# Kernel optimization log

Measured on AMD Instinct MI355X. Metric: run time of the kernel, lower is better.

## Reference

```python
import jax, jax.numpy as jnp
import numpy as np

BETA = 0.25


def setup_inputs() -> dict:
    key = jax.random.key(0)
    k1, k2 = jax.random.split(key)
    z = jax.random.normal(k1, (16, 64, 32, 32), dtype=jnp.float32)
    emb_w = jax.random.normal(k2, (16384, 64), dtype=jnp.float32)
    return {"z": z, "emb_w": emb_w}


def reference(z, emb_w):
    # z: [b, c, h, w] with c == embed_dim; emb_w: [n_embed, embed_dim]
    b, c, h, w = z.shape
    zc = jnp.transpose(z, (0, 2, 3, 1))          # [b, h, w, c]
    zf = zc.reshape(-1, c)                        # [N, c]
    # squared euclidean distances: ||z||^2 - 2 z E^T + ||E||^2  -> [N, n_embed]
    d = (jnp.sum(zf * zf, axis=1, keepdims=True)
         - 2.0 * (zf @ emb_w.T)
         + jnp.sum(emb_w * emb_w, axis=1))
    idx = jnp.argmin(d, axis=1)                   # [N]
    z_q = emb_w[idx].reshape(zc.shape)            # [b, h, w, c]
    # commitment loss (codebook side detached, eval-mode forward)
    loss = BETA * jnp.mean((jax.lax.stop_gradient(z_q) - zc) ** 2)
    # straight-through estimator
    z_q_ste = zc + jax.lax.stop_gradient(z_q - zc)
    z_q_out = jnp.transpose(z_q_ste, (0, 3, 1, 2))  # back to bchw
    return (z_q_out, loss)
```

## Files before the change

kernel.cpp:

```cpp
#include <hip/hip_runtime.h>
#include <math.h>

#define NQ      16384
#define NE      16384
#define DIM     64
#define QB      256
#define CS1     8
#define CPB1    (NE / CS1)
#define CPW1    (CPB1 / 4)
#define NT1     (CPW1 / 32)
#define THREADS 256
#define EPS     0.4f

typedef _Float16 half8  __attribute__((ext_vector_type(8)));
typedef float    f32x4  __attribute__((ext_vector_type(4)));
typedef float    f32x16 __attribute__((ext_vector_type(16)));
typedef unsigned int       uint32;
typedef unsigned short     uint16;
typedef unsigned long long uint64;

typedef union { f32x16 v; f32x4 q[4]; } nvec16;

#define W_NORMS   0
#define W_PM1     16384
#define W_PM2     147456
#define W_PG      278528
#define W_FINALG  344064
#define W_RLIST   360448
#define W_COUNT   376832
#define W_LOSSP   376848
#define W_RKEY    377104
#define W_ZH1     409872
#define W_ZH2     934160
#define W_EH1     1458448
#define W_EH2     1982736

__device__ inline uint32 fmono(float f) {
    uint32 u = __float_as_uint(f);
    return (u & 0x80000000u) ? ~u : (u | 0x80000000u);
}

__global__ __launch_bounds__(THREADS)
void vq_prep(const float* __restrict__ z, const float* __restrict__ emb,
             _Float16* __restrict__ zh1, _Float16* __restrict__ zh2,
             _Float16* __restrict__ eh1, _Float16* __restrict__ eh2,
             float* __restrict__ norms, uint32* __restrict__ count) {
    if (blockIdx.x == 0 && threadIdx.x == 0) *count = 0u;
    if (blockIdx.x < 256) {
        int gid = blockIdx.x * THREADS + threadIdx.x;
        int e = gid >> 2, p = gid & 3;
        const float4* row = reinterpret_cast<const float4*>(emb + (size_t)e * DIM + p * 16);
        float s = 0.f;
#pragma unroll
        for (int i = 0; i < 4; ++i) {
            float4 v = row[i];
            s = fmaf(v.x, v.x, s); s = fmaf(v.y, v.y, s);
            s = fmaf(v.z, v.z, s); s = fmaf(v.w, v.w, s);
            union { _Float16 h[4]; uint2 u; } p1, p2;
            float f[4] = {-2.f * v.x, -2.f * v.y, -2.f * v.z, -2.f * v.w};
#pragma unroll
            for (int j = 0; j < 4; ++j) {
                _Float16 h1 = (_Float16)f[j];
                p1.h[j] = h1;
                p2.h[j] = (_Float16)(f[j] - (float)h1);
            }
            *reinterpret_cast<uint2*>(eh1 + (size_t)e * DIM + p * 16 + i * 4) = p1.u;
            *reinterpret_cast<uint2*>(eh2 + (size_t)e * DIM + p * 16 + i * 4) = p2.u;
        }
        s += __shfl_xor(s, 1, 64);
        s += __shfl_xor(s, 2, 64);
        if (p == 0) norms[e] = s;
    } else {
        int gid = (blockIdx.x - 256) * THREADS + threadIdx.x;
        int n = gid >> 2, p = gid & 3;
        const float* zp = z + (size_t)(n >> 10) * 65536 + (n & 1023) + (size_t)(p * 16) * 1024;
#pragma unroll
        for (int i4 = 0; i4 < 4; ++i4) {
            union { _Float16 h[4]; uint2 u; } p1, p2;
#pragma unroll
            for (int j = 0; j < 4; ++j) {
                float x = zp[(size_t)(i4 * 4 + j) * 1024];
                _Float16 h1 = (_Float16)x;
                p1.h[j] = h1;
                p2.h[j] = (_Float16)(x - (float)h1);
            }
            *reinterpret_cast<uint2*>(zh1 + (size_t)n * DIM + p * 16 + i4 * 4) = p1.u;
            *reinterpret_cast<uint2*>(zh2 + (size_t)n * DIM + p * 16 + i4 * 4) = p2.u;
        }
    }
}

#define LOADT(AS, TL) {                                                            \
    const _Float16* _pa = eh1 + (size_t)(cwbase + (TL) * 32 + q31) * DIM + hi8;    \
    AS[0] = *reinterpret_cast<const half8*>(_pa);                                  \
    AS[1] = *reinterpret_cast<const half8*>(_pa + 16);                             \
    AS[2] = *reinterpret_cast<const half8*>(_pa + 32);                             \
    AS[3] = *reinterpret_cast<const half8*>(_pa + 48); }

#define LOADSN(SN, TL) {                                                           \
    _Pragma("unroll")                                                              \
    for (int k = 0; k < 32; ++k) SN[k] = nrm_s[(TL) * 32 + k]; }

#define MKNS(NS, SN) {                                                             \
    _Pragma("unroll")                                                              \
    for (int j = 0; j < 16; ++j)                                                   \
        NS.v[j] = hi ? SN[(j >> 2) * 8 + 4 + (j & 3)] : SN[(j >> 2) * 8 + (j & 3)]; }

#define COMPUTE(AS, NS, TL) {                                                      \
    const uint32 _tid = (uint32)(TL);                                              \
    _Pragma("unroll")                                                              \
    for (int qg = 0; qg < 8; ++qg) {                                               \
        f32x16 acc;                                                                \
        __builtin_amdgcn_s_setprio(1);                                             \
        acc = __builtin_amdgcn_mfma_f32_32x32x16_f16(AS[0], B[qg][0], NS.v, 0, 0, 0); \
        acc = __builtin_amdgcn_mfma_f32_32x32x16_f16(AS[1], B[qg][1], acc,  0, 0, 0); \
        acc = __builtin_amdgcn_mfma_f32_32x32x16_f16(AS[2], B[qg][2], acc,  0, 0, 0); \
        acc = __builtin_amdgcn_mfma_f32_32x32x16_f16(AS[3], B[qg][3], acc,  0, 0, 0); \
        __builtin_amdgcn_s_setprio(0);                                             \
        float u0 = fminf(fminf(acc[0],  acc[1]),  acc[2]);                         \
        float u1 = fminf(fminf(acc[3],  acc[4]),  acc[5]);                         \
        float u2 = fminf(fminf(acc[6],  acc[7]),  acc[8]);                         \
        float u3 = fminf(fminf(acc[9],  acc[10]), acc[11]);                        \
        float u4 = fminf(fminf(acc[12], acc[13]), acc[14]);                        \
        float v  = fminf(fminf(fminf(u0, u1), u2), fminf(fminf(u3, u4), acc[15])); \
        float nm2 = fminf(m2[qg], fmaxf(v, mv[qg]));              \
        bool lt = v < mv[qg];                             \
        mv[qg] = lt ? v : mv[qg];                                                  \
        mi[qg] = lt ? _tid : mi[qg];                                               \
        m2[qg] = nm2;                                                              \
    } }

__global__ __launch_bounds__(THREADS, 2)
void vq_pass1(const _Float16* __restrict__ zh1, const _Float16* __restrict__ eh1,
              const float* __restrict__ norms,
              float* __restrict__ pm1, float* __restrict__ pm2, uint16* __restrict__ pg) {
    __shared__ float  redv[4][QB];
    __shared__ float  red2[4][QB];
    __shared__ uint32 redg[4][QB];

    const int t    = threadIdx.x;
    const int lane = t & 63;
    const int wave = t >> 6;
    const int q31  = lane & 31;
    const int hi   = lane >> 5;
    const int hi8  = hi * 8;
    const int qbase  = blockIdx.x * QB;
    const int cwbase = blockIdx.y * CPB1 + wave * CPW1;

    const float* nrm_s = norms + (size_t)__builtin_amdgcn_readfirstlane(cwbase);

    half8 B[8][4];
#pragma unroll
    for (int qg = 0; qg < 8; ++qg)
#pragma unroll
        for (int kc = 0; kc < 4; ++kc)
            B[qg][kc] = *reinterpret_cast<const half8*>(
                zh1 + (size_t)(qbase + qg * 32 + q31) * DIM + kc * 16 + hi8);

    float  mv[8], m2[8];
    uint32 mi[8];
#pragma unroll
    for (int q = 0; q < 8; ++q) { mv[q] = INFINITY; m2[q] = INFINITY; mi[q] = 0u; }

    half8 A0[4], A1[4];
    float sn0[32], sn1[32];

    LOADT(A0, 0) LOADSN(sn0, 0)
    for (int tb = 0; tb < NT1; tb += 2) {
        LOADT(A1, tb + 1) LOADSN(sn1, tb + 1)
        {
            nvec16 N0; MKNS(N0, sn0)
            COMPUTE(A0, N0, tb)
        }
        int nx = (tb + 2 < NT1) ? tb + 2 : 0;
        LOADT(A0, nx) LOADSN(sn0, nx)
        {
            nvec16 N1; MKNS(N1, sn1)
            COMPUTE(A1, N1, tb + 1)
        }
    }

    uint32 gi[8];
#pragma unroll
    for (int qg = 0; qg < 8; ++qg)
        gi[qg] = ((uint32)(cwbase >> 5) + mi[qg]) * 2u + (uint32)hi;

#pragma unroll
    for (int qg = 0; qg < 8; ++qg) {
        float  ov = __shfl_xor(mv[qg], 32, 64);
        float  o2 = __shfl_xor(m2[qg], 32, 64);
        uint32 og = (uint32)__shfl_xor((int)gi[qg], 32, 64);
        float nm2 = fminf(fminf(m2[qg], o2), fmaxf(mv[qg], ov));
        if (ov < mv[qg] || (ov == mv[qg] && og < gi[qg])) { mv[qg] = ov; gi[qg] = og; }
        m2[qg] = nm2;
    }
    if (lane < 32) {
#pragma unroll
        for (int qg = 0; qg < 8; ++qg) {
            redv[wave][qg * 32 + lane] = mv[qg];
            red2[wave][qg * 32 + lane] = m2[qg];
            redg[wave][qg * 32 + lane] = gi[qg];
        }
    }
    __syncthreads();

    {
        float  bv = redv[0][t], b2 = red2[0][t];
        uint32 bg = redg[0][t];
#pragma unroll
        for (int w = 1; w < 4; ++w) {
            float v = redv[w][t], s2 = red2[w][t];
            float nm2 = fminf(fminf(b2, s2), fmaxf(bv, v));
            if (v < bv) { bv = v; bg = redg[w][t]; }
            b2 = nm2;
        }
        pm1[(size_t)blockIdx.y * NQ + qbase + t] = bv;
        pm2[(size_t)blockIdx.y * NQ + qbase + t] = b2;
        pg [(size_t)blockIdx.y * NQ + qbase + t] = (uint16)bg;
    }
}

__global__ __launch_bounds__(THREADS)
void vq_select(const float* __restrict__ pm1, const float* __restrict__ pm2,
               const uint16* __restrict__ pg,
               uint32* __restrict__ final_g, uint32* __restrict__ rlist,
               uint32* __restrict__ count, uint64* __restrict__ rkey) {
    const int n = blockIdx.x * THREADS + threadIdx.x;
    float M1 = INFINITY, M2 = INFINITY;
    uint32 G = 0u;
#pragma unroll
    for (int s = 0; s < CS1; ++s) {
        float  m1  = pm1[(size_t)s * NQ + n];
        float  m2s = pm2[(size_t)s * NQ + n];
        uint32 g   = (uint32)pg[(size_t)s * NQ + n];
        float nm2 = fminf(fminf(M2, m2s), fmaxf(M1, m1));
        if (m1 < M1) { M1 = m1; G = g; }
        M2 = nm2;
    }
    rkey[n] = ~0ull;
    if (M2 - M1 > EPS) {
        final_g[n] = G;
    } else {
        final_g[n] = 0xFFFFFFFFu;
        uint32 p = atomicAdd(count, 1u);
        rlist[p] = (uint32)n;
    }
}

__global__ __launch_bounds__(THREADS, 2)
void vq_rescue(const _Float16* __restrict__ zh1, const _Float16* __restrict__ zh2,
               const _Float16* __restrict__ eh1, const _Float16* __restrict__ eh2,
               const float* __restrict__ norms,
               const uint32* __restrict__ rlist, const uint32* __restrict__ countp,
               uint64* __restrict__ rkey) {
    __shared__ float  redv[4][128];
    __shared__ uint32 redg[4][128];

    const uint32 count = *countp;
    const uint32 nch   = (count + 127u) >> 7;
    const int t    = threadIdx.x;
    const int lane = t & 63;
    const int wave = t >> 6;
    const int r15  = lane & 15, hk = lane >> 4;
    const int cy   = blockIdx.x & 15;
    const int rcb  = cy * 1024 + wave * 256;

    for (uint32 cx = (uint32)(blockIdx.x >> 4); cx < nch; cx += 32u) {
        half8 B1[8][2], B2[8][2];
#pragma unroll
        for (int qt = 0; qt < 8; ++qt) {
            uint32 j = cx * 128u + (uint32)(qt * 16 + r15);
            uint32 qid = (j < count) ? rlist[j] : 0u;
#pragma unroll
            for (int kc = 0; kc < 2; ++kc) {
                size_t off = (size_t)qid * DIM + kc * 32 + hk * 8;
                B1[qt][kc] = *reinterpret_cast<const half8*>(zh1 + off);
                B2[qt][kc] = *reinterpret_cast<const half8*>(zh2 + off);
            }
        }

        float  mv[8];
        uint32 mi[8];
#pragma unroll
        for (int q = 0; q < 8; ++q) { mv[q] = INFINITY; mi[q] = 0u; }

        half8 a1[2], a2[2];
        f32x4 nc;
        {
            const _Float16* p1 = eh1 + (size_t)(rcb + r15) * DIM + hk * 8;
            const _Float16* p2 = eh2 + (size_t)(rcb + r15) * DIM + hk * 8;
            a1[0] = *reinterpret_cast<const half8*>(p1);
            a1[1] = *reinterpret_cast<const half8*>(p1 + 32);
            a2[0] = *reinterpret_cast<const half8*>(p2);
            a2[1] = *reinterpret_cast<const half8*>(p2 + 32);
            nc = *reinterpret_cast<const f32x4*>(norms + rcb + hk * 4);
        }

#pragma unroll 2
        for (int tile = 0; tile < 16; ++tile) {
            int nt = (tile + 1 < 16) ? tile + 1 : tile;
            half8 b1[2], b2[2];
            f32x4 nn;
            {
                const _Float16* p1 = eh1 + (size_t)(rcb + nt * 16 + r15) * DIM + hk * 8;
                const _Float16* p2 = eh2 + (size_t)(rcb + nt * 16 + r15) * DIM + hk * 8;
                b1[0] = *reinterpret_cast<const half8*>(p1);
                b1[1] = *reinterpret_cast<const half8*>(p1 + 32);
                b2[0] = *reinterpret_cast<const half8*>(p2);
                b2[1] = *reinterpret_cast<const half8*>(p2 + 32);
                nn = *reinterpret_cast<const f32x4*>(norms + rcb + nt * 16 + hk * 4);
            }

            f32x4 acc[8];
            __builtin_amdgcn_s_setprio(1);
#pragma unroll
            for (int qt = 0; qt < 8; ++qt) {
                acc[qt] = __builtin_amdgcn_mfma_f32_16x16x32_f16(a1[0], B1[qt][0], nc,      0, 0, 0);
                acc[qt] = __builtin_amdgcn_mfma_f32_16x16x32_f16(a1[1], B1[qt][1], acc[qt], 0, 0, 0);
                acc[qt] = __builtin_amdgcn_mfma_f32_16x16x32_f16(a1[0], B2[qt][0], acc[qt], 0, 0, 0);
                acc[qt] = __builtin_amdgcn_mfma_f32_16x16x32_f16(a1[1], B2[qt][1], acc[qt], 0, 0, 0);
                acc[qt] = __builtin_amdgcn_mfma_f32_16x16x32_f16(a2[0], B1[qt][0], acc[qt], 0, 0, 0);
                acc[qt] = __builtin_amdgcn_mfma_f32_16x16x32_f16(a2[1], B1[qt][1], acc[qt], 0, 0, 0);
            }
            __builtin_amdgcn_s_setprio(0);

            const uint32 tid = (uint32)tile;
#pragma unroll
            for (int qt = 0; qt < 8; ++qt) {
                float v = fminf(fminf(fminf(acc[qt][0], acc[qt][1]), acc[qt][2]), acc[qt][3]);
                bool lt = v < mv[qt];
                mv[qt] = lt ? v : mv[qt];
                mi[qt] = lt ? tid : mi[qt];
            }
            a1[0] = b1[0]; a1[1] = b1[1];
            a2[0] = b2[0]; a2[1] = b2[1];
            nc = nn;
        }

        uint32 gi[8];
#pragma unroll
        for (int q = 0; q < 8; ++q)
            gi[q] = (uint32)(rcb >> 2) + (mi[q] << 2) + (uint32)hk;
#pragma unroll
        for (int st = 16; st < 64; st <<= 1) {
#pragma unroll
            for (int q = 0; q < 8; ++q) {
                float  ov = __shfl_xor(mv[q], st, 64);
                uint32 og = (uint32)__shfl_xor((int)gi[q], st, 64);
                if (ov < mv[q] || (ov == mv[q] && og < gi[q])) { mv[q] = ov; gi[q] = og; }
            }
        }
        if (lane < 16) {
#pragma unroll
            for (int qt = 0; qt < 8; ++qt) {
                redv[wave][qt * 16 + lane] = mv[qt];
                redg[wave][qt * 16 + lane] = gi[qt];
            }
        }
        __syncthreads();
        if (t < 128) {
            float  bv = redv[0][t];
            uint32 bg = redg[0][t];
#pragma unroll
            for (int w = 1; w < 4; ++w) {
                float v = redv[w][t];
                if (v < bv) { bv = v; bg = redg[w][t]; }
            }
            uint32 j = cx * 128u + (uint32)t;
            if (j < count) {
                uint64 key = ((uint64)fmono(bv) << 32) | (uint64)bg;
                atomicMin(rkey + rlist[j], key);
            }
        }
        __syncthreads();
    }
}

__global__ __launch_bounds__(THREADS)
void vq_finalize(const float* __restrict__ z,
                 const float* __restrict__ emb,
                 const float* __restrict__ norms,
                 const uint32* __restrict__ final_g,
                 const uint64* __restrict__ rkey,
                 float* __restrict__ out,
                 float* __restrict__ lossp) {
    const int t  = threadIdx.x;
    const int ql = t >> 2, p = t & 3;
    const int n  = blockIdx.x * 64 + ql;
    const int c0 = p * 16;

    uint32 bg = final_g[n];
    if (bg == 0xFFFFFFFFu) {
        uint32 c4 = (uint32)(rkey[n] & 0xFFFFFFFFull) * 4u;
        bg = (c4 >> 5) * 2u + ((c4 >> 2) & 1u);
    }
    const int gbase = (int)((bg >> 1) * 32u + (bg & 1u) * 4u);

    const float* zp = z + (size_t)(n >> 10) * 65536 + (n & 1023);
    float zq[16];
#pragma unroll
    for (int c = 0; c < 16; ++c) zq[c] = zp[(size_t)(c0 + c) * 1024];

    float dp[16];
#pragma unroll
    for (int j = 0; j < 16; ++j) {
        int code = gbase + (j & 3) + 8 * (j >> 2);
        const float4* er = reinterpret_cast<const float4*>(emb + (size_t)code * DIM + c0);
        float d = 0.f;
#pragma unroll
        for (int i = 0; i < 4; ++i) {
            float4 e4 = er[i];
            d = fmaf(e4.x, zq[i * 4 + 0], d);
            d = fmaf(e4.y, zq[i * 4 + 1], d);
            d = fmaf(e4.z, zq[i * 4 + 2], d);
            d = fmaf(e4.w, zq[i * 4 + 3], d);
        }
        dp[j] = d;
    }
#pragma unroll
    for (int st = 1; st < 4; st <<= 1) {
#pragma unroll
        for (int j = 0; j < 16; ++j) dp[j] += __shfl_xor(dp[j], st, 64);
    }

    f32x4 nr[4];
#pragma unroll
    for (int k = 0; k < 4; ++k)
        nr[k] = *reinterpret_cast<const f32x4*>(norms + gbase + k * 8);

    float bs = INFINITY;
    uint32 bi = 0u;
#pragma unroll
    for (int j = 0; j < 16; ++j) {
        float s = fmaf(-2.f, dp[j], nr[j >> 2][j & 3]);
        uint32 code = (uint32)(gbase + (j & 3) + 8 * (j >> 2));
        if (s < bs) { bs = s; bi = code; }
    }

    const float* ew = emb + (size_t)bi * DIM + c0;
    float* op = out + (size_t)(n >> 10) * 65536 + (n & 1023);

    float ls = 0.f;
#pragma unroll
    for (int c = 0; c < 16; ++c) {
        float e = ew[c];
        op[(size_t)(c0 + c) * 1024] = e;
        float d = e - zq[c];
        ls = fmaf(d, d, ls);
    }

#pragma unroll
    for (int off = 32; off > 0; off >>= 1) ls += __shfl_down(ls, off, 64);
    __shared__ float wsum[THREADS / 64];
    if ((t & 63) == 0) wsum[t >> 6] = ls;
    __syncthreads();
    if (t == 0) {
        float s = 0.f;
#pragma unroll
        for (int w = 0; w < THREADS / 64; ++w) s += wsum[w];
        lossp[blockIdx.x] = s;
    }
}

__global__ __launch_bounds__(64)
void vq_loss_final(const float* __restrict__ lossp, float* __restrict__ out) {
    float v = 0.f;
#pragma unroll
    for (int k = 0; k < 4; ++k) v += lossp[threadIdx.x + k * 64];
#pragma unroll
    for (int off = 32; off > 0; off >>= 1) v += __shfl_down(v, off, 64);
    if (threadIdx.x == 0)
        out[1048576] = 0.25f * v / 1048576.0f;
}

extern "C" void kernel_launch(void* const* d_in, const int* in_sizes, int n_in,
                              void* d_out, int out_size, void* d_ws, size_t ws_size,
                              hipStream_t stream) {
    const float* z   = (const float*)d_in[0];
    const float* emb = (const float*)d_in[1];
    float* out = (float*)d_out;

    float* ws = (float*)d_ws;
    float*     norms   = ws + W_NORMS;
    float*     pm1     = ws + W_PM1;
    float*     pm2     = ws + W_PM2;
    uint16*    pg      = (uint16*)(ws + W_PG);
    uint32*    final_g = (uint32*)(ws + W_FINALG);
    uint32*    rlist   = (uint32*)(ws + W_RLIST);
    uint32*    count   = (uint32*)(ws + W_COUNT);
    float*     lossp   = ws + W_LOSSP;
    uint64*    rkey    = (uint64*)(ws + W_RKEY);
    _Float16*  zh1     = (_Float16*)(ws + W_ZH1);
    _Float16*  zh2     = (_Float16*)(ws + W_ZH2);
    _Float16*  eh1     = (_Float16*)(ws + W_EH1);
    _Float16*  eh2     = (_Float16*)(ws + W_EH2);

    vq_prep<<<512, THREADS, 0, stream>>>(z, emb, zh1, zh2, eh1, eh2, norms, count);

    dim3 g1(NQ / QB, CS1);
    vq_pass1<<<g1, THREADS, 0, stream>>>(zh1, eh1, norms, pm1, pm2, pg);

    vq_select<<<NQ / THREADS, THREADS, 0, stream>>>(pm1, pm2, pg, final_g, rlist, count, rkey);

    vq_rescue<<<512, THREADS, 0, stream>>>(zh1, zh2, eh1, eh2, norms, rlist, count, rkey);

    vq_finalize<<<NQ / 64, THREADS, 0, stream>>>(z, emb, norms, final_g, rkey, out, lossp);
    vq_loss_final<<<1, 64, 0, stream>>>(lossp, out);
}
```

Baseline: 78.86 us.

## Share codebook tiles across waves via swizzled LDS in pass1

Restructures vq_pass1 so that each of the four waves handles a different 256-query slice while all waves share the same codebook tile. The tile is staged cooperatively into a swizzled LDS buffer with a register prefetch, replacing the per-wave global loads of separate codebook chunks. This cuts redundant global/L2 traffic for the codebook, and the grid changes to 16x32 blocks with more codebook splits. In exchange it adds two barriers per tile and writes 4x more partial minima, so vq_select now reduces over 32 splits.

```diff
diff --git a/kernel.cpp b/kernel.cpp
--- a/kernel.cpp
+++ b/kernel.cpp
@@ -4,11 +4,10 @@
 #define NQ      16384
 #define NE      16384
 #define DIM     64
-#define QB      256
-#define CS1     8
+#define QBB     1024
+#define CS1     32
 #define CPB1    (NE / CS1)
-#define CPW1    (CPB1 / 4)
-#define NT1     (CPW1 / 32)
+#define NT1     (CPB1 / 32)
 #define THREADS 256
 #define EPS     0.4f
 
@@ -23,17 +22,17 @@
 
 #define W_NORMS   0
 #define W_PM1     16384
-#define W_PM2     147456
-#define W_PG      278528
-#define W_FINALG  344064
-#define W_RLIST   360448
-#define W_COUNT   376832
-#define W_LOSSP   376848
-#define W_RKEY    377104
-#define W_ZH1     409872
-#define W_ZH2     934160
-#define W_EH1     1458448
-#define W_EH2     1982736
+#define W_PM2     540672
+#define W_PG      1064960
+#define W_FINALG  1327104
+#define W_RLIST   1343488
+#define W_COUNT   1359872
+#define W_LOSSP   1359888
+#define W_RKEY    1360144
+#define W_ZH1     1392912
+#define W_ZH2     1917200
+#define W_EH1     2441488
+#define W_EH2     2965776
 
 __device__ inline uint32 fmono(float f) {
     uint32 u = __float_as_uint(f);
@@ -89,13 +88,6 @@
         }
     }
 }
-
-#define LOADT(AS, TL) {                                                            \
-    const _Float16* _pa = eh1 + (size_t)(cwbase + (TL) * 32 + q31) * DIM + hi8;    \
-    AS[0] = *reinterpret_cast<const half8*>(_pa);                                  \
-    AS[1] = *reinterpret_cast<const half8*>(_pa + 16);                             \
-    AS[2] = *reinterpret_cast<const half8*>(_pa + 32);                             \
-    AS[3] = *reinterpret_cast<const half8*>(_pa + 48); }
 
 #define LOADSN(SN, TL) {                                                           \
     _Pragma("unroll")                                                              \
@@ -134,9 +126,7 @@
 void vq_pass1(const _Float16* __restrict__ zh1, const _Float16* __restrict__ eh1,
               const float* __restrict__ norms,
               float* __restrict__ pm1, float* __restrict__ pm2, uint16* __restrict__ pg) {
-    __shared__ float  redv[4][QB];
-    __shared__ float  red2[4][QB];
-    __shared__ uint32 redg[4][QB];
+    __shared__ __align__(16) _Float16 lA[2048];
 
     const int t    = threadIdx.x;
     const int lane = t & 63;
@@ -144,10 +134,9 @@
     const int q31  = lane & 31;
     const int hi   = lane >> 5;
     const int hi8  = hi * 8;
-    const int qbase  = blockIdx.x * QB;
-    const int cwbase = blockIdx.y * CPB1 + wave * CPW1;
-
-    const float* nrm_s = norms + (size_t)__builtin_amdgcn_readfirstlane(cwbase);
+    const int qbase = blockIdx.x * QBB + wave * 256;
+    const int cbase = blockIdx.y * CPB1;
+    const float* nrm_s = norms + cbase;
 
     half8 B[8][4];
 #pragma unroll
@@ -157,33 +146,41 @@
             B[qg][kc] = *reinterpret_cast<const half8*>(
                 zh1 + (size_t)(qbase + qg * 32 + q31) * DIM + kc * 16 + hi8);
 
+    int rd0 = q31 * 128 + (((0 * 2 + hi) ^ (q31 & 7)) << 4);
+    int rd1 = q31 * 128 + (((1 * 2 + hi) ^ (q31 & 7)) << 4);
+    int rd2 = q31 * 128 + (((2 * 2 + hi) ^ (q31 & 7)) << 4);
+    int rd3 = q31 * 128 + (((3 * 2 + hi) ^ (q31 & 7)) << 4);
+    const int wrh = (t >> 3) * 64 + (((t & 7) ^ ((t >> 3) & 7)) * 8);
+
     float  mv[8], m2[8];
     uint32 mi[8];
 #pragma unroll
     for (int q = 0; q < 8; ++q) { mv[q] = INFINITY; m2[q] = INFINITY; mi[q] = 0u; }
 
-    half8 A0[4], A1[4];
-    float sn0[32], sn1[32];
-
-    LOADT(A0, 0) LOADSN(sn0, 0)
-    for (int tb = 0; tb < NT1; tb += 2) {
-        LOADT(A1, tb + 1) LOADSN(sn1, tb + 1)
-        {
-            nvec16 N0; MKNS(N0, sn0)
-            COMPUTE(A0, N0, tb)
-        }
-        int nx = (tb + 2 < NT1) ? tb + 2 : 0;
-        LOADT(A0, nx) LOADSN(sn0, nx)
-        {
-            nvec16 N1; MKNS(N1, sn1)
-            COMPUTE(A1, N1, tb + 1)
-        }
+    half8 g = *reinterpret_cast<const half8*>(eh1 + (size_t)cbase * DIM + t * 8);
+
+    for (int tl = 0; tl < NT1; ++tl) {
+        __syncthreads();
+        *reinterpret_cast<half8*>(lA + wrh) = g;
+        if (tl + 1 < NT1)
+            g = *reinterpret_cast<const half8*>(
+                eh1 + (size_t)cbase * DIM + (tl + 1) * 2048 + t * 8);
+        float sn[32];
+        LOADSN(sn, tl)
+        __syncthreads();
+        nvec16 N; MKNS(N, sn)
+        half8 A[4];
+        A[0] = *reinterpret_cast<const half8*>(reinterpret_cast<const unsigned char*>(lA) + rd0);
+        A[1] = *reinterpret_cast<const half8*>(reinterpret_cast<const unsigned char*>(lA) + rd1);
+        A[2] = *reinterpret_cast<const half8*>(reinterpret_cast<const unsigned char*>(lA) + rd2);
+        A[3] = *reinterpret_cast<const half8*>(reinterpret_cast<const unsigned char*>(lA) + rd3);
+        COMPUTE(A, N, tl)
     }
 
     uint32 gi[8];
 #pragma unroll
     for (int qg = 0; qg < 8; ++qg)
-        gi[qg] = ((uint32)(cwbase >> 5) + mi[qg]) * 2u + (uint32)hi;
+        gi[qg] = ((uint32)(blockIdx.y * NT1) + mi[qg]) * 2u + (uint32)hi;
 
 #pragma unroll
     for (int qg = 0; qg < 8; ++qg) {
@@ -197,26 +194,11 @@
     if (lane < 32) {
 #pragma unroll
         for (int qg = 0; qg < 8; ++qg) {
-            redv[wave][qg * 32 + lane] = mv[qg];
-            red2[wave][qg * 32 + lane] = m2[qg];
-            redg[wave][qg * 32 + lane] = gi[qg];
-        }
-    }
-    __syncthreads();
-
-    {
-        float  bv = redv[0][t], b2 = red2[0][t];
-        uint32 bg = redg[0][t];
-#pragma unroll
-        for (int w = 1; w < 4; ++w) {
-            float v = redv[w][t], s2 = red2[w][t];
-            float nm2 = fminf(fminf(b2, s2), fmaxf(bv, v));
-            if (v < bv) { bv = v; bg = redg[w][t]; }
-            b2 = nm2;
-        }
-        pm1[(size_t)blockIdx.y * NQ + qbase + t] = bv;
-        pm2[(size_t)blockIdx.y * NQ + qbase + t] = b2;
-        pg [(size_t)blockIdx.y * NQ + qbase + t] = (uint16)bg;
+            size_t o = (size_t)blockIdx.y * NQ + qbase + qg * 32 + lane;
+            pm1[o] = mv[qg];
+            pm2[o] = m2[qg];
+            pg [o] = (uint16)gi[qg];
+        }
     }
 }
 
@@ -228,7 +210,7 @@
     const int n = blockIdx.x * THREADS + threadIdx.x;
     float M1 = INFINITY, M2 = INFINITY;
     uint32 G = 0u;
-#pragma unroll
+#pragma unroll 8
     for (int s = 0; s < CS1; ++s) {
         float  m1  = pm1[(size_t)s * NQ + n];
         float  m2s = pm2[(size_t)s * NQ + n];
@@ -497,7 +479,7 @@
 
     vq_prep<<<512, THREADS, 0, stream>>>(z, emb, zh1, zh2, eh1, eh2, norms, count);
 
-    dim3 g1(NQ / QB, CS1);
+    dim3 g1(NQ / QBB, CS1);
     vq_pass1<<<g1, THREADS, 0, stream>>>(zh1, eh1, norms, pm1, pm2, pg);
 
     vq_select<<<NQ / THREADS, THREADS, 0, stream>>>(pm1, pm2, pg, final_g, rlist, count, rkey);
```

Result: slower. 81.56 us (median of 3 runs) (+3.4%).
